# Kernel optimization log

Measured on AMD Instinct MI355X. Metric: run time of the kernel, lower is better.

Reference implementation:

```python
import jax, jax.numpy as jnp
import numpy as np

SQ, SK, D = 8192, 8192, 128

def setup_inputs() -> dict:
    k = jax.random.key(0)
    kq, kk, kv = jax.random.split(k, 3)
    query = jax.random.normal(kq, (SQ, D), dtype=jnp.float32)
    key = jax.random.normal(kk, (SK, D), dtype=jnp.float32)
    value = jax.random.normal(kv, (SK, D), dtype=jnp.float32)
    return {"query": query, "key": key, "value": value}

def reference(query, key, value):
    # attn_weights = dot_general(q, k, contract last dims) -> [Sq, Sk]
    attn_weights = jnp.einsum('qd,kd->qk', query, key)
    # softmax over key dims (second half of attn_weights dims)
    attn_weights = jax.nn.softmax(attn_weights, axis=-1)
    # dropout is identity: train=False -> deterministic
    # y = dot_general(attn_weights, value, contract key dims) -> [Sq, Dv]
    y = jnp.einsum('qk,kd->qd', attn_weights, value)
    return y
```

## Files before the change

### kernel.cpp

```cpp
#include <hip/hip_runtime.h>
#include <hip/hip_bf16.h>
#include <stdint.h>

#define SQ 8192
#define SK 8192
#define DH 128
#define NIT 32
#define L2E 1.4426950408889634f
#define CB 40.0f

typedef __attribute__((ext_vector_type(8))) _Float16 f16x8;
typedef __attribute__((ext_vector_type(8))) short bf16x8;
typedef __attribute__((ext_vector_type(16))) float f32x16;
typedef __attribute__((ext_vector_type(4))) short s16x4;
typedef __attribute__((ext_vector_type(4))) unsigned int u32x4;

__device__ __forceinline__ short f2h(float f) {
  _Float16 h = (_Float16)f;
  return __builtin_bit_cast(short, h);
}
__device__ __forceinline__ short f2bf(float f) {
  uint32_t u = __builtin_bit_cast(uint32_t, f);
  u = (u + 0x7FFFu + ((u >> 16) & 1u)) >> 16;
  return (short)u;
}

__global__ __launch_bounds__(256) void prep_kernel(const float* __restrict__ K,
                                                   const float* __restrict__ V,
                                                   short* __restrict__ Kimg,
                                                   short* __restrict__ Vimg) {
  __shared__ short T[32][136];
  const int tid = threadIdx.x;
  if (blockIdx.x < 256) {
    const int kb = blockIdx.x;
#pragma unroll
    for (int i = 0; i < 2; ++i) {
      int ci = i * 256 + tid;
      int kc = ci >> 6, lane = ci & 63;
      int key = kb * 32 + (lane & 31);
      int k0 = kc * 16 + (lane >> 5) * 8;
      const float* src = K + (size_t)key * DH + k0;
      float4 a = *(const float4*)src;
      float4 b = *(const float4*)(src + 4);
      s16x4 o0, o1;
      o0.x = f2h(a.x); o0.y = f2h(a.y); o0.z = f2h(a.z); o0.w = f2h(a.w);
      o1.x = f2h(b.x); o1.y = f2h(b.y); o1.z = f2h(b.z); o1.w = f2h(b.w);
      s16x4* dst = (s16x4*)(Kimg + (size_t)kb * 4096 + ci * 8);
      dst[0] = o0; dst[1] = o1;
    }
  } else {
    const int kb = blockIdx.x - 256;
#pragma unroll
    for (int i = 0; i < 4; ++i) {
      int fi = i * 256 + tid;
      int key = fi >> 5;
      int dc = (fi & 31) * 4;
      float4 v = ((const float4*)V)[(size_t)(kb * 32 + key) * (DH / 4) + (fi & 31)];
      T[key][dc + 0] = f2bf(v.x); T[key][dc + 1] = f2bf(v.y);
      T[key][dc + 2] = f2bf(v.z); T[key][dc + 3] = f2bf(v.w);
    }
    __syncthreads();
#pragma unroll
    for (int i = 0; i < 2; ++i) {
      int ci = i * 256 + tid;
      int lane = ci & 63;
      int g = ci >> 6;
      int dt = g & 3, ks = g >> 2;
      int base = ks * 16 + (lane >> 5) * 4;
      int d = dt * 32 + (lane & 31);
      s16x4 o0, o1;
      o0.x = T[base + 0][d]; o0.y = T[base + 1][d];
      o0.z = T[base + 2][d]; o0.w = T[base + 3][d];
      o1.x = T[base + 8][d]; o1.y = T[base + 9][d];
      o1.z = T[base + 10][d]; o1.w = T[base + 11][d];
      s16x4* dst = (s16x4*)(Vimg + (size_t)kb * 4096 + ci * 8);
      dst[0] = o0; dst[1] = o1;
    }
  }
}

__global__ __launch_bounds__(512, 2) void attn_kernel(const float* __restrict__ Q,
                                                      const short* __restrict__ Kimg,
                                                      const short* __restrict__ Vimg,
                                                      float* __restrict__ out) {
  __shared__ __align__(16) char smem[67584];
  const int tid = threadIdx.x;
  const int w = tid >> 6;
  const int lane = tid & 63;
  const int half = lane >> 5;
  const int l32 = lane & 31;
  const int qrow0 = blockIdx.x * 32;

  f16x8 qf[8];
  {
    const float* qp = Q + (size_t)(qrow0 + l32) * DH + half * 8;
#pragma unroll
    for (int kc = 0; kc < 8; ++kc) {
      float4 a = *(const float4*)(qp + kc * 16);
      float4 b = *(const float4*)(qp + kc * 16 + 4);
      f16x8 h;
      h[0] = (_Float16)a.x; h[1] = (_Float16)a.y; h[2] = (_Float16)a.z; h[3] = (_Float16)a.w;
      h[4] = (_Float16)b.x; h[5] = (_Float16)b.y; h[6] = (_Float16)b.z; h[7] = (_Float16)b.w;
      qf[kc] = h;
    }
  }

  f32x16 of[4];
#pragma unroll
  for (int dt = 0; dt < 4; ++dt)
#pragma unroll
    for (int c = 0; c < 16; ++c) of[dt][c] = 0.f;
  float l_lane = 0.f;

  f16x8 kf[8];
  bf16x8 vf[8];

  {
    const short* kp = Kimg + (size_t)w * 4096;
    const short* vp = Vimg + (size_t)w * 4096;
#pragma unroll
    for (int kc = 0; kc < 8; ++kc) kf[kc] = *(const f16x8*)(kp + kc * 512 + lane * 8);
#pragma unroll
    for (int g = 0; g < 8; ++g) vf[g] = *(const bf16x8*)(vp + g * 512 + lane * 8);
  }

  for (int t = 0; t < NIT; ++t) {
    f32x16 sacc;
#pragma unroll
    for (int c = 0; c < 16; ++c) sacc[c] = 0.f;
#pragma unroll
    for (int kc = 0; kc < 8; ++kc)
      sacc = __builtin_amdgcn_mfma_f32_32x32x16_f16(kf[kc], qf[kc], sacc, 0, 0, 0);

    if (t + 1 < NIT) {
      const short* kp = Kimg + (size_t)((t + 1) * 8 + w) * 4096;
#pragma unroll
      for (int kc = 0; kc < 8; ++kc) kf[kc] = *(const f16x8*)(kp + kc * 512 + lane * 8);
    }

    u32x4 pav0, pav1;
#pragma unroll
    for (int r = 0; r < 4; ++r) {
      float pA = __builtin_amdgcn_exp2f(fmaf(sacc[2 * r], L2E, -CB));
      float pB = __builtin_amdgcn_exp2f(fmaf(sacc[2 * r + 1], L2E, -CB));
      float pC = __builtin_amdgcn_exp2f(fmaf(sacc[8 + 2 * r], L2E, -CB));
      float pD = __builtin_amdgcn_exp2f(fmaf(sacc[8 + 2 * r + 1], L2E, -CB));
      l_lane += (pA + pB) + (pC + pD);
      uint32_t uA = __builtin_bit_cast(uint32_t, pA); uA += 0x7FFFu + ((uA >> 16) & 1u);
      uint32_t uB = __builtin_bit_cast(uint32_t, pB); uB += 0x7FFFu + ((uB >> 16) & 1u);
      uint32_t uC = __builtin_bit_cast(uint32_t, pC); uC += 0x7FFFu + ((uC >> 16) & 1u);
      uint32_t uD = __builtin_bit_cast(uint32_t, pD); uD += 0x7FFFu + ((uD >> 16) & 1u);
      pav0[r] = __builtin_amdgcn_perm(uB, uA, 0x07060302u);
      pav1[r] = __builtin_amdgcn_perm(uD, uC, 0x07060302u);
    }
    bf16x8 pa0 = __builtin_bit_cast(bf16x8, pav0);
    bf16x8 pa1 = __builtin_bit_cast(bf16x8, pav1);

#pragma unroll
    for (int dt = 0; dt < 4; ++dt) {
      of[dt] = __builtin_amdgcn_mfma_f32_32x32x16_bf16(pa0, vf[dt], of[dt], 0, 0, 0);
      of[dt] = __builtin_amdgcn_mfma_f32_32x32x16_bf16(pa1, vf[4 + dt], of[dt], 0, 0, 0);
    }

    if (t + 1 < NIT) {
      const short* vp = Vimg + (size_t)((t + 1) * 8 + w) * 4096;
#pragma unroll
      for (int g = 0; g < 8; ++g) vf[g] = *(const bf16x8*)(vp + g * 512 + lane * 8);
    }
  }

  float l_tot = l_lane + __shfl_xor(l_lane, 32);

  __syncthreads();
  float* mO = (float*)smem;
  float* R = mO + (w & 3) * 4224;
  if (w < 4) {
#pragma unroll
    for (int c = 0; c < 16; ++c) {
      const int row = (c & 3) + 8 * (c >> 2) + 4 * half;
      float* br = R + row * 132;
#pragma unroll
      for (int dt = 0; dt < 4; ++dt) br[dt * 32 + l32] = of[dt][c];
    }
    if (half == 0) R[l32 * 132 + 128] = l_tot;
  }
  __syncthreads();
  if (w >= 4) {
#pragma unroll
    for (int c = 0; c < 16; ++c) {
      const int row = (c & 3) + 8 * (c >> 2) + 4 * half;
      float* br = R + row * 132;
#pragma unroll
      for (int dt = 0; dt < 4; ++dt) br[dt * 32 + l32] += of[dt][c];
    }
    if (half == 0) R[l32 * 132 + 128] += l_tot;
  }
  __syncthreads();
  {
    const int row = tid >> 4;
    const int cg = tid & 15;
    float den = mO[row * 132 + 128] + mO[4224 + row * 132 + 128] +
                mO[8448 + row * 132 + 128] + mO[12672 + row * 132 + 128];
    float inv = 1.f / den;
    float4 s0 = {0.f, 0.f, 0.f, 0.f}, s1 = {0.f, 0.f, 0.f, 0.f};
#pragma unroll
    for (int rg = 0; rg < 4; ++rg) {
      const float* p = mO + rg * 4224 + row * 132 + cg * 8;
      float4 a = *(const float4*)p;
      float4 b = *(const float4*)(p + 4);
      s0.x += a.x; s0.y += a.y; s0.z += a.z; s0.w += a.w;
      s1.x += b.x; s1.y += b.y; s1.z += b.z; s1.w += b.w;
    }
    s0.x *= inv; s0.y *= inv; s0.z *= inv; s0.w *= inv;
    s1.x *= inv; s1.y *= inv; s1.z *= inv; s1.w *= inv;
    float* op = out + (size_t)(qrow0 + row) * DH + cg * 8;
    *(float4*)op = s0;
    *(float4*)(op + 4) = s1;
  }
}

extern "C" void kernel_launch(void* const* d_in, const int* in_sizes, int n_in,
                              void* d_out, int out_size, void* d_ws, size_t ws_size,
                              hipStream_t stream) {
  const float* Q = (const float*)d_in[0];
  const float* K = (const float*)d_in[1];
  const float* V = (const float*)d_in[2];
  float* out = (float*)d_out;
  short* Kimg = (short*)d_ws;
  short* Vimg = (short*)d_ws + (size_t)SK * DH;
  prep_kernel<<<512, 256, 0, stream>>>(K, V, Kimg, Vimg);
  attn_kernel<<<SQ / 32, 512, 0, stream>>>(Q, Kimg, Vimg, out);
}
```

Baseline: 112.7 us.

## Split key loop across twelve waves per block with zero-padded key blocks

Each attention block now runs 12 waves (768 threads) instead of 8, so every wave walks 22 key blocks instead of 32. The key count is padded from 256 to 264 blocks, and the padding is written as zeros by the prep kernel. The cross-wave reduction gains a third accumulate round. Zero K rows give exp(-CB) contributions to the softmax denominator, but their V rows are zero. The change drops the occupancy hint of 2 blocks per CU and adds padding work and an extra reduction/sync round.

```diff
diff --git a/kernel.cpp b/kernel.cpp
--- a/kernel.cpp
+++ b/kernel.cpp
@@ -5,7 +5,8 @@
 #define SQ 8192
 #define SK 8192
 #define DH 128
-#define NIT 32
+#define NKB 264
+#define NIT 22
 #define L2E 1.4426950408889634f
 #define CB 40.0f
 
@@ -31,58 +32,66 @@
                                                    short* __restrict__ Vimg) {
   __shared__ short T[32][136];
   const int tid = threadIdx.x;
-  if (blockIdx.x < 256) {
+  if (blockIdx.x < NKB) {
     const int kb = blockIdx.x;
+    const bool pad = (kb >= 256);
 #pragma unroll
     for (int i = 0; i < 2; ++i) {
       int ci = i * 256 + tid;
-      int kc = ci >> 6, lane = ci & 63;
-      int key = kb * 32 + (lane & 31);
-      int k0 = kc * 16 + (lane >> 5) * 8;
-      const float* src = K + (size_t)key * DH + k0;
-      float4 a = *(const float4*)src;
-      float4 b = *(const float4*)(src + 4);
-      s16x4 o0, o1;
-      o0.x = f2h(a.x); o0.y = f2h(a.y); o0.z = f2h(a.z); o0.w = f2h(a.w);
-      o1.x = f2h(b.x); o1.y = f2h(b.y); o1.z = f2h(b.z); o1.w = f2h(b.w);
+      s16x4 o0 = {0, 0, 0, 0}, o1 = {0, 0, 0, 0};
+      if (!pad) {
+        int kc = ci >> 6, lane = ci & 63;
+        int key = kb * 32 + (lane & 31);
+        int k0 = kc * 16 + (lane >> 5) * 8;
+        const float* src = K + (size_t)key * DH + k0;
+        float4 a = *(const float4*)src;
+        float4 b = *(const float4*)(src + 4);
+        o0.x = f2h(a.x); o0.y = f2h(a.y); o0.z = f2h(a.z); o0.w = f2h(a.w);
+        o1.x = f2h(b.x); o1.y = f2h(b.y); o1.z = f2h(b.z); o1.w = f2h(b.w);
+      }
       s16x4* dst = (s16x4*)(Kimg + (size_t)kb * 4096 + ci * 8);
       dst[0] = o0; dst[1] = o1;
     }
   } else {
-    const int kb = blockIdx.x - 256;
-#pragma unroll
-    for (int i = 0; i < 4; ++i) {
-      int fi = i * 256 + tid;
-      int key = fi >> 5;
-      int dc = (fi & 31) * 4;
-      float4 v = ((const float4*)V)[(size_t)(kb * 32 + key) * (DH / 4) + (fi & 31)];
-      T[key][dc + 0] = f2bf(v.x); T[key][dc + 1] = f2bf(v.y);
-      T[key][dc + 2] = f2bf(v.z); T[key][dc + 3] = f2bf(v.w);
-    }
-    __syncthreads();
+    const int kb = blockIdx.x - NKB;
+    const bool pad = (kb >= 256);
+    if (!pad) {
+#pragma unroll
+      for (int i = 0; i < 4; ++i) {
+        int fi = i * 256 + tid;
+        int key = fi >> 5;
+        int dc = (fi & 31) * 4;
+        float4 v = ((const float4*)V)[(size_t)(kb * 32 + key) * (DH / 4) + (fi & 31)];
+        T[key][dc + 0] = f2bf(v.x); T[key][dc + 1] = f2bf(v.y);
+        T[key][dc + 2] = f2bf(v.z); T[key][dc + 3] = f2bf(v.w);
+      }
+      __syncthreads();
+    }
 #pragma unroll
     for (int i = 0; i < 2; ++i) {
       int ci = i * 256 + tid;
-      int lane = ci & 63;
-      int g = ci >> 6;
-      int dt = g & 3, ks = g >> 2;
-      int base = ks * 16 + (lane >> 5) * 4;
-      int d = dt * 32 + (lane & 31);
-      s16x4 o0, o1;
-      o0.x = T[base + 0][d]; o0.y = T[base + 1][d];
-      o0.z = T[base + 2][d]; o0.w = T[base + 3][d];
-      o1.x = T[base + 8][d]; o1.y = T[base + 9][d];
-      o1.z = T[base + 10][d]; o1.w = T[base + 11][d];
+      s16x4 o0 = {0, 0, 0, 0}, o1 = {0, 0, 0, 0};
+      if (!pad) {
+        int lane = ci & 63;
+        int g = ci >> 6;
+        int dt = g & 3, ks = g >> 2;
+        int base = ks * 16 + (lane >> 5) * 4;
+        int d = dt * 32 + (lane & 31);
+        o0.x = T[base + 0][d]; o0.y = T[base + 1][d];
+        o0.z = T[base + 2][d]; o0.w = T[base + 3][d];
+        o1.x = T[base + 8][d]; o1.y = T[base + 9][d];
+        o1.z = T[base + 10][d]; o1.w = T[base + 11][d];
+      }
       s16x4* dst = (s16x4*)(Vimg + (size_t)kb * 4096 + ci * 8);
       dst[0] = o0; dst[1] = o1;
     }
   }
 }
 
-__global__ __launch_bounds__(512, 2) void attn_kernel(const float* __restrict__ Q,
-                                                      const short* __restrict__ Kimg,
-                                                      const short* __restrict__ Vimg,
-                                                      float* __restrict__ out) {
+__global__ __launch_bounds__(768) void attn_kernel(const float* __restrict__ Q,
+                                                   const short* __restrict__ Kimg,
+                                                   const short* __restrict__ Vimg,
+                                                   float* __restrict__ out) {
   __shared__ __align__(16) char smem[67584];
   const int tid = threadIdx.x;
   const int w = tid >> 6;
@@ -133,7 +142,7 @@
       sacc = __builtin_amdgcn_mfma_f32_32x32x16_f16(kf[kc], qf[kc], sacc, 0, 0, 0);
 
     if (t + 1 < NIT) {
-      const short* kp = Kimg + (size_t)((t + 1) * 8 + w) * 4096;
+      const short* kp = Kimg + (size_t)((t + 1) * 12 + w) * 4096;
 #pragma unroll
       for (int kc = 0; kc < 8; ++kc) kf[kc] = *(const f16x8*)(kp + kc * 512 + lane * 8);
     }
@@ -163,7 +172,7 @@
     }
 
     if (t + 1 < NIT) {
-      const short* vp = Vimg + (size_t)((t + 1) * 8 + w) * 4096;
+      const short* vp = Vimg + (size_t)((t + 1) * 12 + w) * 4096;
 #pragma unroll
       for (int g = 0; g < 8; ++g) vf[g] = *(const bf16x8*)(vp + g * 512 + lane * 8);
     }
@@ -174,29 +183,33 @@
   __syncthreads();
   float* mO = (float*)smem;
   float* R = mO + (w & 3) * 4224;
-  if (w < 4) {
-#pragma unroll
-    for (int c = 0; c < 16; ++c) {
-      const int row = (c & 3) + 8 * (c >> 2) + 4 * half;
-      float* br = R + row * 132;
-#pragma unroll
-      for (int dt = 0; dt < 4; ++dt) br[dt * 32 + l32] = of[dt][c];
-    }
-    if (half == 0) R[l32 * 132 + 128] = l_tot;
-  }
-  __syncthreads();
-  if (w >= 4) {
-#pragma unroll
-    for (int c = 0; c < 16; ++c) {
-      const int row = (c & 3) + 8 * (c >> 2) + 4 * half;
-      float* br = R + row * 132;
-#pragma unroll
-      for (int dt = 0; dt < 4; ++dt) br[dt * 32 + l32] += of[dt][c];
-    }
-    if (half == 0) R[l32 * 132 + 128] += l_tot;
-  }
-  __syncthreads();
-  {
+  const int wg = w >> 2;
+#pragma unroll
+  for (int round = 0; round < 3; ++round) {
+    if (wg == round) {
+      if (round == 0) {
+#pragma unroll
+        for (int c = 0; c < 16; ++c) {
+          const int row = (c & 3) + 8 * (c >> 2) + 4 * half;
+          float* br = R + row * 132;
+#pragma unroll
+          for (int dt = 0; dt < 4; ++dt) br[dt * 32 + l32] = of[dt][c];
+        }
+        if (half == 0) R[l32 * 132 + 128] = l_tot;
+      } else {
+#pragma unroll
+        for (int c = 0; c < 16; ++c) {
+          const int row = (c & 3) + 8 * (c >> 2) + 4 * half;
+          float* br = R + row * 132;
+#pragma unroll
+          for (int dt = 0; dt < 4; ++dt) br[dt * 32 + l32] += of[dt][c];
+        }
+        if (half == 0) R[l32 * 132 + 128] += l_tot;
+      }
+    }
+    __syncthreads();
+  }
+  if (tid < 512) {
     const int row = tid >> 4;
     const int cg = tid & 15;
     float den = mO[row * 132 + 128] + mO[4224 + row * 132 + 128] +
@@ -227,7 +240,7 @@
   const float* V = (const float*)d_in[2];
   float* out = (float*)d_out;
   short* Kimg = (short*)d_ws;
-  short* Vimg = (short*)d_ws + (size_t)SK * DH;
-  prep_kernel<<<512, 256, 0, stream>>>(K, V, Kimg, Vimg);
-  attn_kernel<<<SQ / 32, 512, 0, stream>>>(Q, Kimg, Vimg, out);
-}
+  short* Vimg = (short*)d_ws + (size_t)NKB * 4096;
+  prep_kernel<<<2 * NKB, 256, 0, stream>>>(K, V, Kimg, Vimg);
+  attn_kernel<<<SQ / 32, 768, 0, stream>>>(Q, Kimg, Vimg, out);
+}
```

Result: slower. 144.5 us (+28.2%).

## Software-pipeline QK^T of next tile with softmax and PV of current tile

Applied to the files above, without the earlier changes.

Restructures the key loop into a two-stage ping-pong: the QK^T MFMAs for the next key tile are issued while the exp/pack and PV MFMAs of the current tile run, with double-buffered K fragments and two score accumulators. Launch bounds drop from 2 to 1 block per CU to allow the extra registers. The aim is to hide the softmax VALU latency behind matrix work. It gives up occupancy, which reduces latency hiding across waves.

```diff
diff --git a/kernel.cpp b/kernel.cpp
--- a/kernel.cpp
+++ b/kernel.cpp
@@ -79,7 +79,28 @@
   }
 }
 
-__global__ __launch_bounds__(512, 2) void attn_kernel(const float* __restrict__ Q,
+__device__ __forceinline__ void soft_pack(const f32x16& sacc, float& l_lane,
+                                          bf16x8& pa0, bf16x8& pa1) {
+  u32x4 pav0, pav1;
+#pragma unroll
+  for (int r = 0; r < 4; ++r) {
+    float pA = __builtin_amdgcn_exp2f(fmaf(sacc[2 * r], L2E, -CB));
+    float pB = __builtin_amdgcn_exp2f(fmaf(sacc[2 * r + 1], L2E, -CB));
+    float pC = __builtin_amdgcn_exp2f(fmaf(sacc[8 + 2 * r], L2E, -CB));
+    float pD = __builtin_amdgcn_exp2f(fmaf(sacc[8 + 2 * r + 1], L2E, -CB));
+    l_lane += (pA + pB) + (pC + pD);
+    uint32_t uA = __builtin_bit_cast(uint32_t, pA); uA += 0x7FFFu + ((uA >> 16) & 1u);
+    uint32_t uB = __builtin_bit_cast(uint32_t, pB); uB += 0x7FFFu + ((uB >> 16) & 1u);
+    uint32_t uC = __builtin_bit_cast(uint32_t, pC); uC += 0x7FFFu + ((uC >> 16) & 1u);
+    uint32_t uD = __builtin_bit_cast(uint32_t, pD); uD += 0x7FFFu + ((uD >> 16) & 1u);
+    pav0[r] = __builtin_amdgcn_perm(uB, uA, 0x07060302u);
+    pav1[r] = __builtin_amdgcn_perm(uD, uC, 0x07060302u);
+  }
+  pa0 = __builtin_bit_cast(bf16x8, pav0);
+  pa1 = __builtin_bit_cast(bf16x8, pav1);
+}
+
+__global__ __launch_bounds__(512, 1) void attn_kernel(const float* __restrict__ Q,
                                                       const short* __restrict__ Kimg,
                                                       const short* __restrict__ Vimg,
                                                       float* __restrict__ out) {
@@ -112,58 +133,71 @@
     for (int c = 0; c < 16; ++c) of[dt][c] = 0.f;
   float l_lane = 0.f;
 
-  f16x8 kf[8];
+  f16x8 kfA[8], kfB[8];
   bf16x8 vf[8];
 
   {
     const short* kp = Kimg + (size_t)w * 4096;
     const short* vp = Vimg + (size_t)w * 4096;
 #pragma unroll
-    for (int kc = 0; kc < 8; ++kc) kf[kc] = *(const f16x8*)(kp + kc * 512 + lane * 8);
+    for (int kc = 0; kc < 8; ++kc) kfA[kc] = *(const f16x8*)(kp + kc * 512 + lane * 8);
 #pragma unroll
     for (int g = 0; g < 8; ++g) vf[g] = *(const bf16x8*)(vp + g * 512 + lane * 8);
   }
-
-  for (int t = 0; t < NIT; ++t) {
-    f32x16 sacc;
-#pragma unroll
-    for (int c = 0; c < 16; ++c) sacc[c] = 0.f;
-#pragma unroll
-    for (int kc = 0; kc < 8; ++kc)
-      sacc = __builtin_amdgcn_mfma_f32_32x32x16_f16(kf[kc], qf[kc], sacc, 0, 0, 0);
-
-    if (t + 1 < NIT) {
-      const short* kp = Kimg + (size_t)((t + 1) * 8 + w) * 4096;
-#pragma unroll
-      for (int kc = 0; kc < 8; ++kc) kf[kc] = *(const f16x8*)(kp + kc * 512 + lane * 8);
-    }
-
-    u32x4 pav0, pav1;
-#pragma unroll
-    for (int r = 0; r < 4; ++r) {
-      float pA = __builtin_amdgcn_exp2f(fmaf(sacc[2 * r], L2E, -CB));
-      float pB = __builtin_amdgcn_exp2f(fmaf(sacc[2 * r + 1], L2E, -CB));
-      float pC = __builtin_amdgcn_exp2f(fmaf(sacc[8 + 2 * r], L2E, -CB));
-      float pD = __builtin_amdgcn_exp2f(fmaf(sacc[8 + 2 * r + 1], L2E, -CB));
-      l_lane += (pA + pB) + (pC + pD);
-      uint32_t uA = __builtin_bit_cast(uint32_t, pA); uA += 0x7FFFu + ((uA >> 16) & 1u);
-      uint32_t uB = __builtin_bit_cast(uint32_t, pB); uB += 0x7FFFu + ((uB >> 16) & 1u);
-      uint32_t uC = __builtin_bit_cast(uint32_t, pC); uC += 0x7FFFu + ((uC >> 16) & 1u);
-      uint32_t uD = __builtin_bit_cast(uint32_t, pD); uD += 0x7FFFu + ((uD >> 16) & 1u);
-      pav0[r] = __builtin_amdgcn_perm(uB, uA, 0x07060302u);
-      pav1[r] = __builtin_amdgcn_perm(uD, uC, 0x07060302u);
-    }
-    bf16x8 pa0 = __builtin_bit_cast(bf16x8, pav0);
-    bf16x8 pa1 = __builtin_bit_cast(bf16x8, pav1);
-
-#pragma unroll
-    for (int dt = 0; dt < 4; ++dt) {
-      of[dt] = __builtin_amdgcn_mfma_f32_32x32x16_bf16(pa0, vf[dt], of[dt], 0, 0, 0);
-      of[dt] = __builtin_amdgcn_mfma_f32_32x32x16_bf16(pa1, vf[4 + dt], of[dt], 0, 0, 0);
-    }
-
-    if (t + 1 < NIT) {
-      const short* vp = Vimg + (size_t)((t + 1) * 8 + w) * 4096;
+  f32x16 saccA, saccB;
+#pragma unroll
+  for (int c = 0; c < 16; ++c) saccA[c] = 0.f;
+#pragma unroll
+  for (int kc = 0; kc < 8; ++kc)
+    saccA = __builtin_amdgcn_mfma_f32_32x32x16_f16(kfA[kc], qf[kc], saccA, 0, 0, 0);
+  {
+    const short* kp = Kimg + (size_t)(8 + w) * 4096;
+#pragma unroll
+    for (int kc = 0; kc < 8; ++kc) kfB[kc] = *(const f16x8*)(kp + kc * 512 + lane * 8);
+  }
+
+  for (int tt = 0; tt < NIT / 2; ++tt) {
+    const int t0 = 2 * tt, t1 = 2 * tt + 1;
+    {
+      bf16x8 pa0, pa1;
+      soft_pack(saccA, l_lane, pa0, pa1);
+#pragma unroll
+      for (int c = 0; c < 16; ++c) saccB[c] = 0.f;
+#pragma unroll
+      for (int kc = 0; kc < 8; ++kc)
+        saccB = __builtin_amdgcn_mfma_f32_32x32x16_f16(kfB[kc], qf[kc], saccB, 0, 0, 0);
+#pragma unroll
+      for (int dt = 0; dt < 4; ++dt) {
+        of[dt] = __builtin_amdgcn_mfma_f32_32x32x16_bf16(pa0, vf[dt], of[dt], 0, 0, 0);
+        of[dt] = __builtin_amdgcn_mfma_f32_32x32x16_bf16(pa1, vf[4 + dt], of[dt], 0, 0, 0);
+      }
+      const int tk = (t0 + 2 < NIT) ? t0 + 2 : NIT - 1;
+      const short* kp = Kimg + (size_t)(tk * 8 + w) * 4096;
+#pragma unroll
+      for (int kc = 0; kc < 8; ++kc) kfA[kc] = *(const f16x8*)(kp + kc * 512 + lane * 8);
+      const short* vp = Vimg + (size_t)(t1 * 8 + w) * 4096;
+#pragma unroll
+      for (int g = 0; g < 8; ++g) vf[g] = *(const bf16x8*)(vp + g * 512 + lane * 8);
+    }
+    {
+      bf16x8 pa0, pa1;
+      soft_pack(saccB, l_lane, pa0, pa1);
+#pragma unroll
+      for (int c = 0; c < 16; ++c) saccA[c] = 0.f;
+#pragma unroll
+      for (int kc = 0; kc < 8; ++kc)
+        saccA = __builtin_amdgcn_mfma_f32_32x32x16_f16(kfA[kc], qf[kc], saccA, 0, 0, 0);
+#pragma unroll
+      for (int dt = 0; dt < 4; ++dt) {
+        of[dt] = __builtin_amdgcn_mfma_f32_32x32x16_bf16(pa0, vf[dt], of[dt], 0, 0, 0);
+        of[dt] = __builtin_amdgcn_mfma_f32_32x32x16_bf16(pa1, vf[4 + dt], of[dt], 0, 0, 0);
+      }
+      const int tk = (t1 + 2 < NIT) ? t1 + 2 : NIT - 1;
+      const short* kp = Kimg + (size_t)(tk * 8 + w) * 4096;
+#pragma unroll
+      for (int kc = 0; kc < 8; ++kc) kfB[kc] = *(const f16x8*)(kp + kc * 512 + lane * 8);
+      const int tv = (t0 + 2 < NIT) ? t0 + 2 : NIT - 1;
+      const short* vp = Vimg + (size_t)(tv * 8 + w) * 4096;
 #pragma unroll
       for (int g = 0; g < 8; ++g) vf[g] = *(const bf16x8*)(vp + g * 512 + lane * 8);
     }
```

Result: slower. 169.3 us (+50.3%).

## Split keys across block pairs and merge partial outputs in separate kernel

Applied to the files above, without the earlier changes.

Adds a key-split attention kernel. Each block covers 64 query rows over half of the keys, using 2 query subtiles × 4 key stripes of waves. It writes partial outputs normalized and stored as bf16, plus their row sums, to workspace. A merge kernel then combines the two halves using weights from the row sums. The split is meant to change how work and K/V reuse are spread across blocks. In exchange it adds an extra launch, extra global traffic and bf16 rounding of the partial outputs. The old kernel is kept as a fallback when the workspace is too small.

```diff
diff --git a/kernel.cpp b/kernel.cpp
--- a/kernel.cpp
+++ b/kernel.cpp
@@ -5,7 +5,6 @@
 #define SQ 8192
 #define SK 8192
 #define DH 128
-#define NIT 32
 #define L2E 1.4426950408889634f
 #define CB 40.0f
 
@@ -23,6 +22,10 @@
   uint32_t u = __builtin_bit_cast(uint32_t, f);
   u = (u + 0x7FFFu + ((u >> 16) & 1u)) >> 16;
   return (short)u;
+}
+__device__ __forceinline__ float bf2f(short s) {
+  uint32_t u = ((uint32_t)(uint16_t)s) << 16;
+  return __builtin_bit_cast(float, u);
 }
 
 __global__ __launch_bounds__(256) void prep_kernel(const float* __restrict__ K,
@@ -79,10 +82,45 @@
   }
 }
 
-__global__ __launch_bounds__(512, 2) void attn_kernel(const float* __restrict__ Q,
-                                                      const short* __restrict__ Kimg,
-                                                      const short* __restrict__ Vimg,
-                                                      float* __restrict__ out) {
+__device__ __forceinline__ void soft_pack(const f32x16& sacc, float& l_lane,
+                                          bf16x8& pa0, bf16x8& pa1) {
+  u32x4 pav0, pav1;
+#pragma unroll
+  for (int r = 0; r < 4; ++r) {
+    float pA = __builtin_amdgcn_exp2f(fmaf(sacc[2 * r], L2E, -CB));
+    float pB = __builtin_amdgcn_exp2f(fmaf(sacc[2 * r + 1], L2E, -CB));
+    float pC = __builtin_amdgcn_exp2f(fmaf(sacc[8 + 2 * r], L2E, -CB));
+    float pD = __builtin_amdgcn_exp2f(fmaf(sacc[8 + 2 * r + 1], L2E, -CB));
+    l_lane += (pA + pB) + (pC + pD);
+    uint32_t uA = __builtin_bit_cast(uint32_t, pA); uA += 0x7FFFu + ((uA >> 16) & 1u);
+    uint32_t uB = __builtin_bit_cast(uint32_t, pB); uB += 0x7FFFu + ((uB >> 16) & 1u);
+    uint32_t uC = __builtin_bit_cast(uint32_t, pC); uC += 0x7FFFu + ((uC >> 16) & 1u);
+    uint32_t uD = __builtin_bit_cast(uint32_t, pD); uD += 0x7FFFu + ((uD >> 16) & 1u);
+    pav0[r] = __builtin_amdgcn_perm(uB, uA, 0x07060302u);
+    pav1[r] = __builtin_amdgcn_perm(uD, uC, 0x07060302u);
+  }
+  pa0 = __builtin_bit_cast(bf16x8, pav0);
+  pa1 = __builtin_bit_cast(bf16x8, pav1);
+}
+
+__device__ __forceinline__ void load_qf(const float* __restrict__ Q, int qrow,
+                                        int half, f16x8* qf) {
+  const float* qp = Q + (size_t)qrow * DH + half * 8;
+#pragma unroll
+  for (int kc = 0; kc < 8; ++kc) {
+    float4 a = *(const float4*)(qp + kc * 16);
+    float4 b = *(const float4*)(qp + kc * 16 + 4);
+    f16x8 h;
+    h[0] = (_Float16)a.x; h[1] = (_Float16)a.y; h[2] = (_Float16)a.z; h[3] = (_Float16)a.w;
+    h[4] = (_Float16)b.x; h[5] = (_Float16)b.y; h[6] = (_Float16)b.z; h[7] = (_Float16)b.w;
+    qf[kc] = h;
+  }
+}
+
+__global__ __launch_bounds__(512, 1) void attn_r9(const float* __restrict__ Q,
+                                                  const short* __restrict__ Kimg,
+                                                  const short* __restrict__ Vimg,
+                                                  float* __restrict__ out) {
   __shared__ __align__(16) char smem[67584];
   const int tid = threadIdx.x;
   const int w = tid >> 6;
@@ -92,18 +130,7 @@
   const int qrow0 = blockIdx.x * 32;
 
   f16x8 qf[8];
-  {
-    const float* qp = Q + (size_t)(qrow0 + l32) * DH + half * 8;
-#pragma unroll
-    for (int kc = 0; kc < 8; ++kc) {
-      float4 a = *(const float4*)(qp + kc * 16);
-      float4 b = *(const float4*)(qp + kc * 16 + 4);
-      f16x8 h;
-      h[0] = (_Float16)a.x; h[1] = (_Float16)a.y; h[2] = (_Float16)a.z; h[3] = (_Float16)a.w;
-      h[4] = (_Float16)b.x; h[5] = (_Float16)b.y; h[6] = (_Float16)b.z; h[7] = (_Float16)b.w;
-      qf[kc] = h;
-    }
-  }
+  load_qf(Q, qrow0 + l32, half, qf);
 
   f32x16 of[4];
 #pragma unroll
@@ -114,7 +141,6 @@
 
   f16x8 kf[8];
   bf16x8 vf[8];
-
   {
     const short* kp = Kimg + (size_t)w * 4096;
     const short* vp = Vimg + (size_t)w * 4096;
@@ -124,45 +150,26 @@
     for (int g = 0; g < 8; ++g) vf[g] = *(const bf16x8*)(vp + g * 512 + lane * 8);
   }
 
-  for (int t = 0; t < NIT; ++t) {
+  for (int t = 0; t < 32; ++t) {
     f32x16 sacc;
 #pragma unroll
     for (int c = 0; c < 16; ++c) sacc[c] = 0.f;
 #pragma unroll
     for (int kc = 0; kc < 8; ++kc)
       sacc = __builtin_amdgcn_mfma_f32_32x32x16_f16(kf[kc], qf[kc], sacc, 0, 0, 0);
-
-    if (t + 1 < NIT) {
+    if (t + 1 < 32) {
       const short* kp = Kimg + (size_t)((t + 1) * 8 + w) * 4096;
 #pragma unroll
       for (int kc = 0; kc < 8; ++kc) kf[kc] = *(const f16x8*)(kp + kc * 512 + lane * 8);
     }
-
-    u32x4 pav0, pav1;
-#pragma unroll
-    for (int r = 0; r < 4; ++r) {
-      float pA = __builtin_amdgcn_exp2f(fmaf(sacc[2 * r], L2E, -CB));
-      float pB = __builtin_amdgcn_exp2f(fmaf(sacc[2 * r + 1], L2E, -CB));
-      float pC = __builtin_amdgcn_exp2f(fmaf(sacc[8 + 2 * r], L2E, -CB));
-      float pD = __builtin_amdgcn_exp2f(fmaf(sacc[8 + 2 * r + 1], L2E, -CB));
-      l_lane += (pA + pB) + (pC + pD);
-      uint32_t uA = __builtin_bit_cast(uint32_t, pA); uA += 0x7FFFu + ((uA >> 16) & 1u);
-      uint32_t uB = __builtin_bit_cast(uint32_t, pB); uB += 0x7FFFu + ((uB >> 16) & 1u);
-      uint32_t uC = __builtin_bit_cast(uint32_t, pC); uC += 0x7FFFu + ((uC >> 16) & 1u);
-      uint32_t uD = __builtin_bit_cast(uint32_t, pD); uD += 0x7FFFu + ((uD >> 16) & 1u);
-      pav0[r] = __builtin_amdgcn_perm(uB, uA, 0x07060302u);
-      pav1[r] = __builtin_amdgcn_perm(uD, uC, 0x07060302u);
-    }
-    bf16x8 pa0 = __builtin_bit_cast(bf16x8, pav0);
-    bf16x8 pa1 = __builtin_bit_cast(bf16x8, pav1);
-
+    bf16x8 pa0, pa1;
+    soft_pack(sacc, l_lane, pa0, pa1);
 #pragma unroll
     for (int dt = 0; dt < 4; ++dt) {
       of[dt] = __builtin_amdgcn_mfma_f32_32x32x16_bf16(pa0, vf[dt], of[dt], 0, 0, 0);
       of[dt] = __builtin_amdgcn_mfma_f32_32x32x16_bf16(pa1, vf[4 + dt], of[dt], 0, 0, 0);
     }
-
-    if (t + 1 < NIT) {
+    if (t + 1 < 32) {
       const short* vp = Vimg + (size_t)((t + 1) * 8 + w) * 4096;
 #pragma unroll
       for (int g = 0; g < 8; ++g) vf[g] = *(const bf16x8*)(vp + g * 512 + lane * 8);
@@ -219,6 +226,143 @@
   }
 }
 
+__global__ __launch_bounds__(512, 1) void attn_ks(const float* __restrict__ Q,
+                                                  const short* __restrict__ Kimg,
+                                                  const short* __restrict__ Vimg,
+                                                  short* __restrict__ Opart,
+                                                  float* __restrict__ Lpart) {
+  __shared__ __align__(16) char smem[33792];
+  const int tid = threadIdx.x;
+  const int w = tid >> 6;
+  const int lane = tid & 63;
+  const int half = lane >> 5;
+  const int l32 = lane & 31;
+  const int qsub = w & 1;
+  const int stripe = w >> 1;
+  const int qt = blockIdx.x >> 1;
+  const int khalf = blockIdx.x & 1;
+  const int qrow0 = qt * 64 + qsub * 32;
+  const int kb0 = khalf * 128 + stripe;
+
+  f16x8 qf[8];
+  load_qf(Q, qrow0 + l32, half, qf);
+
+  f32x16 of[4];
+#pragma unroll
+  for (int dt = 0; dt < 4; ++dt)
+#pragma unroll
+    for (int c = 0; c < 16; ++c) of[dt][c] = 0.f;
+  float l_lane = 0.f;
+
+  f16x8 kf[8];
+  bf16x8 vf[8];
+  {
+    const short* kp = Kimg + (size_t)kb0 * 4096;
+    const short* vp = Vimg + (size_t)kb0 * 4096;
+#pragma unroll
+    for (int kc = 0; kc < 8; ++kc) kf[kc] = *(const f16x8*)(kp + kc * 512 + lane * 8);
+#pragma unroll
+    for (int g = 0; g < 8; ++g) vf[g] = *(const bf16x8*)(vp + g * 512 + lane * 8);
+  }
+
+  for (int t = 0; t < 32; ++t) {
+    f32x16 sacc;
+#pragma unroll
+    for (int c = 0; c < 16; ++c) sacc[c] = 0.f;
+#pragma unroll
+    for (int kc = 0; kc < 8; ++kc)
+      sacc = __builtin_amdgcn_mfma_f32_32x32x16_f16(kf[kc], qf[kc], sacc, 0, 0, 0);
+    if (t + 1 < 32) {
+      const short* kp = Kimg + (size_t)(kb0 + (t + 1) * 4) * 4096;
+#pragma unroll
+      for (int kc = 0; kc < 8; ++kc) kf[kc] = *(const f16x8*)(kp + kc * 512 + lane * 8);
+    }
+    bf16x8 pa0, pa1;
+    soft_pack(sacc, l_lane, pa0, pa1);
+#pragma unroll
+    for (int dt = 0; dt < 4; ++dt) {
+      of[dt] = __builtin_amdgcn_mfma_f32_32x32x16_bf16(pa0, vf[dt], of[dt], 0, 0, 0);
+      of[dt] = __builtin_amdgcn_mfma_f32_32x32x16_bf16(pa1, vf[4 + dt], of[dt], 0, 0, 0);
+    }
+    if (t + 1 < 32) {
+      const short* vp = Vimg + (size_t)(kb0 + (t + 1) * 4) * 4096;
+#pragma unroll
+      for (int g = 0; g < 8; ++g) vf[g] = *(const bf16x8*)(vp + g * 512 + lane * 8);
+    }
+  }
+
+  float l_tot = l_lane + __shfl_xor(l_lane, 32);
+
+  __syncthreads();
+  float* mO = (float*)smem;
+  float* R = mO + qsub * 4224;
+#pragma unroll
+  for (int round = 0; round < 4; ++round) {
+    if (stripe == round) {
+      if (round == 0) {
+#pragma unroll
+        for (int c = 0; c < 16; ++c) {
+          const int row = (c & 3) + 8 * (c >> 2) + 4 * half;
+          float* br = R + row * 132;
+#pragma unroll
+          for (int dt = 0; dt < 4; ++dt) br[dt * 32 + l32] = of[dt][c];
+        }
+        if (half == 0) R[l32 * 132 + 128] = l_tot;
+      } else {
+#pragma unroll
+        for (int c = 0; c < 16; ++c) {
+          const int row = (c & 3) + 8 * (c >> 2) + 4 * half;
+          float* br = R + row * 132;
+#pragma unroll
+          for (int dt = 0; dt < 4; ++dt) br[dt * 32 + l32] += of[dt][c];
+        }
+        if (half == 0) R[l32 * 132 + 128] += l_tot;
+      }
+    }
+    __syncthreads();
+  }
+
+  {
+    const int row = tid >> 3;
+    const int c0 = (tid & 7) * 16;
+    const float* Rr = mO + (row >> 5) * 4224 + (row & 31) * 132;
+    float l = Rr[128];
+    float inv = 1.f / l;
+    short* dst = Opart + (size_t)blockIdx.x * 8192 + row * 128 + c0;
+    bf16x8 o0, o1;
+#pragma unroll
+    for (int j = 0; j < 8; ++j) o0[j] = f2bf(Rr[c0 + j] * inv);
+#pragma unroll
+    for (int j = 0; j < 8; ++j) o1[j] = f2bf(Rr[c0 + 8 + j] * inv);
+    *(bf16x8*)dst = o0;
+    *(bf16x8*)(dst + 8) = o1;
+    if ((tid & 7) == 0) Lpart[blockIdx.x * 64 + row] = l;
+  }
+}
+
+__global__ __launch_bounds__(256) void merge_kernel(const short* __restrict__ Opart,
+                                                    const float* __restrict__ Lpart,
+                                                    float* __restrict__ out) {
+  int idx = blockIdx.x * 256 + threadIdx.x;
+  int q = idx >> 5;
+  int c4 = (idx & 31) * 4;
+  int qt = q >> 6, r = q & 63;
+  const short* A = Opart + (size_t)(2 * qt) * 8192 + r * 128 + c4;
+  const short* B = Opart + (size_t)(2 * qt + 1) * 8192 + r * 128 + c4;
+  float l0 = Lpart[(2 * qt) * 64 + r];
+  float l1 = Lpart[(2 * qt + 1) * 64 + r];
+  float inv = 1.f / (l0 + l1);
+  float w0 = l0 * inv, w1 = l1 * inv;
+  s16x4 a = *(const s16x4*)A;
+  s16x4 b = *(const s16x4*)B;
+  float4 o;
+  o.x = bf2f(a.x) * w0 + bf2f(b.x) * w1;
+  o.y = bf2f(a.y) * w0 + bf2f(b.y) * w1;
+  o.z = bf2f(a.z) * w0 + bf2f(b.z) * w1;
+  o.w = bf2f(a.w) * w0 + bf2f(b.w) * w1;
+  ((float4*)out)[idx] = o;
+}
+
 extern "C" void kernel_launch(void* const* d_in, const int* in_sizes, int n_in,
                               void* d_out, int out_size, void* d_ws, size_t ws_size,
                               hipStream_t stream) {
@@ -226,8 +370,17 @@
   const float* K = (const float*)d_in[1];
   const float* V = (const float*)d_in[2];
   float* out = (float*)d_out;
-  short* Kimg = (short*)d_ws;
-  short* Vimg = (short*)d_ws + (size_t)SK * DH;
+  char* base = (char*)d_ws;
+  short* Kimg = (short*)base;
+  short* Vimg = (short*)(base + 2097152);
+  short* Opart = (short*)(base + 4194304);
+  float* Lpart = (float*)(base + 8388608);
+  const size_t NEED = 8388608 + 65536;
   prep_kernel<<<512, 256, 0, stream>>>(K, V, Kimg, Vimg);
-  attn_kernel<<<SQ / 32, 512, 0, stream>>>(Q, Kimg, Vimg, out);
-}
+  if (ws_size >= NEED) {
+    attn_ks<<<256, 512, 0, stream>>>(Q, Kimg, Vimg, Opart, Lpart);
+    merge_kernel<<<1024, 256, 0, stream>>>(Opart, Lpart, out);
+  } else {
+    attn_r9<<<SQ / 32, 512, 0, stream>>>(Q, Kimg, Vimg, out);
+  }
+}
```

Result: slower. 116.5 us (+3.4%).
